# Performance work log

Hardware: AMD Instinct MI355X
Metric: run time of the kernel (lower is better)

The kernel has to match this reference:

```python
import math
import jax, jax.numpy as jnp
import numpy as np

W_BITS = 8
A_BITS = 8
N_HEADS = 16

def fake_quant(x, bits):
    # symmetric per-tensor fake quantization with straight-through estimator
    if bits >= 32:
        return x
    qmax = float(2 ** (bits - 1) - 1)
    scale = jnp.maximum(jnp.max(jnp.abs(x)) / qmax, 1e-8)
    q = jnp.round(x / scale) * scale
    return x + jax.lax.stop_gradient(q - x)

def qlinear(x, W, b):
    # QuantizeLinear: quantize activations (a_bits) and weights (w_bits), then y = x @ W^T + b
    xq = fake_quant(x, A_BITS)
    Wq = fake_quant(W, W_BITS)
    return jnp.einsum('bsd,ed->bse', xq, Wq) + b

def setup_inputs() -> dict:
    key = jax.random.key(0)
    B, S, D = 2, 2048, 1024
    ks = jax.random.split(key, 6)
    inp = {
        'hidden_states': jax.random.normal(ks[0], (B, S, D), dtype=jnp.float32),
        'attention_mask': jnp.ones((B, S), dtype=jnp.float32),
        'Wq': 0.02 * jax.random.normal(ks[1], (D, D), dtype=jnp.float32),
        'bq': jnp.zeros((D,), dtype=jnp.float32),
        'Wk': 0.02 * jax.random.normal(ks[2], (D, D), dtype=jnp.float32),
        'bk': jnp.zeros((D,), dtype=jnp.float32),
        'Wv': 0.02 * jax.random.normal(ks[3], (D, D), dtype=jnp.float32),
        'bv': jnp.zeros((D,), dtype=jnp.float32),
        'Wo': 0.02 * jax.random.normal(ks[4], (D, D), dtype=jnp.float32),
        'bo': jnp.zeros((D,), dtype=jnp.float32),
    }
    return inp

def reference(hidden_states, attention_mask, Wq, bq, Wk, bk, Wv, bv, Wo, bo):
    B, S, D = hidden_states.shape
    H = N_HEADS
    hd = D // H

    q = qlinear(hidden_states, Wq, bq).reshape(B, S, H, hd)
    k = qlinear(hidden_states, Wk, bk).reshape(B, S, H, hd)
    v = qlinear(hidden_states, Wv, bv).reshape(B, S, H, hd)

    # scores: [B, H, Sq, Sk]
    scores = jnp.einsum('bqhd,bkhd->bhqk', q, k) / math.sqrt(hd)
    mask_bias = (1.0 - attention_mask)[:, None, None, :] * -10000.0
    scores = scores + mask_bias
    probs = jax.nn.softmax(scores, axis=-1)

    attn = jnp.einsum('bhqk,bkhd->bqhd', probs, v).reshape(B, S, D)
    return qlinear(attn, Wo, bo)
```

## Files before the change

### kernel.cpp

```cpp
#include <hip/hip_runtime.h>
#include <cstddef>
#include <cstdint>

constexpr int Bb = 2, Ss = 2048, Dd = 1024, Hh = 16, HD = 64;
constexpr int Mm = Bb * Ss;

typedef int v4i __attribute__((ext_vector_type(4)));
typedef __bf16 bf16x8 __attribute__((ext_vector_type(8)));
typedef float f32x16 __attribute__((ext_vector_type(16)));

#define QPOSTMUL 0.18033688f
#define MASKBIAS -14426.950408f

__device__ __forceinline__ float qscale(float amax) {
    return fmaxf(amax / 127.0f, 1e-8f);
}

__device__ __forceinline__ unsigned short bf16rtn(float x) {
    __bf16 b = (__bf16)x;
    return __builtin_bit_cast(unsigned short, b);
}

__device__ __forceinline__ void bf16split(float x, unsigned short& hi, unsigned short& lo) {
    unsigned u = __float_as_uint(x);
    unsigned h = (u + 0x7fffu + ((u >> 16) & 1u)) >> 16;
    hi = (unsigned short)h;
    float r = x - __uint_as_float(h << 16);
    unsigned v = __float_as_uint(r);
    lo = (unsigned short)((v + 0x7fffu + ((v >> 16) & 1u)) >> 16);
}

__global__ void amax_all(const float4* __restrict__ hidden,
                         const float4* __restrict__ w0, const float4* __restrict__ w1,
                         const float4* __restrict__ w2, const float4* __restrict__ w3,
                         unsigned* __restrict__ slots) {
    const float4* src; int n4, slot, bx, nb;
    if (blockIdx.x < 256) { src = hidden; n4 = Mm * Dd / 4; slot = 0; bx = blockIdx.x; nb = 256; }
    else {
        int w = (blockIdx.x - 256) >> 4; bx = (blockIdx.x - 256) & 15; nb = 16;
        src = w == 0 ? w0 : w == 1 ? w1 : w == 2 ? w2 : w3;
        n4 = Dd * Dd / 4; slot = 1 + w;
    }
    float m = 0.f;
    for (int i = bx * blockDim.x + threadIdx.x; i < n4; i += nb * blockDim.x) {
        float4 v = src[i];
        m = fmaxf(m, fmaxf(fmaxf(fabsf(v.x), fabsf(v.y)), fmaxf(fabsf(v.z), fabsf(v.w))));
    }
    #pragma unroll
    for (int off = 32; off > 0; off >>= 1) m = fmaxf(m, __shfl_down(m, off, 64));
    __shared__ float sm[4];
    int lane = threadIdx.x & 63, wid = threadIdx.x >> 6;
    if (lane == 0) sm[wid] = m;
    __syncthreads();
    if (threadIdx.x == 0) {
        float mm = fmaxf(fmaxf(sm[0], sm[1]), fmaxf(sm[2], sm[3]));
        atomicMax(slots + slot, __float_as_uint(mm));
    }
}

__global__ void quant_all(const float* __restrict__ hidden,
                          const float* __restrict__ w0, const float* __restrict__ w1,
                          const float* __restrict__ w2, const float* __restrict__ w3,
                          const float* __restrict__ amax,
                          char* __restrict__ hq8, char* __restrict__ Wall8) {
    const float* x; char* y; int n4, slot, bx, nb;
    if (blockIdx.x < 1024) { x = hidden; y = hq8; n4 = Mm * Dd / 4; slot = 0; bx = blockIdx.x; nb = 1024; }
    else {
        int w = (blockIdx.x - 1024) >> 5; bx = (blockIdx.x - 1024) & 31; nb = 32;
        x = w == 0 ? w0 : w == 1 ? w1 : w == 2 ? w2 : w3;
        y = Wall8 + ((size_t)w << 20);
        n4 = Dd * Dd / 4; slot = 1 + w;
    }
    float s = qscale(amax[slot]);
    const float4* x4 = (const float4*)x;
    char4* y4 = (char4*)y;
    for (int i = bx * blockDim.x + threadIdx.x; i < n4; i += nb * blockDim.x) {
        float4 v = x4[i];
        char4 q;
        q.x = (char)(int)rintf(v.x / s);
        q.y = (char)(int)rintf(v.y / s);
        q.z = (char)(int)rintf(v.z / s);
        q.w = (char)(int)rintf(v.w / s);
        y4[i] = q;
    }
}

__global__ void quant_a(const float* __restrict__ x, char* __restrict__ y,
                        const float* __restrict__ amax, int n4) {
    float s = qscale(amax[0]);
    int stride = gridDim.x * blockDim.x;
    const float4* x4 = (const float4*)x;
    char4* y4 = (char4*)y;
    for (int i = blockIdx.x * blockDim.x + threadIdx.x; i < n4; i += stride) {
        float4 v = x4[i];
        char4 q;
        q.x = (char)(int)rintf(v.x / s);
        q.y = (char)(int)rintf(v.y / s);
        q.z = (char)(int)rintf(v.z / s);
        q.w = (char)(int)rintf(v.w / s);
        y4[i] = q;
    }
}

#define GLOAD_LDS16(g, l) __builtin_amdgcn_global_load_lds( \
    (const __attribute__((address_space(1))) unsigned int*)(g), \
    (__attribute__((address_space(3))) unsigned int*)(l), 16, 0, 0)

__device__ __forceinline__ void gemm_i8_core(const char* __restrict__ A, const char* __restrict__ Bw,
                                             int bm, int bn, int K, int t,
                                             char* At, char* Bt, v4i acc[4][4]) {
    const int lane = t & 63, w = t >> 6;
    const int wm = (w >> 1) * 64, wn = (w & 1) * 64;
    const int lr = lane & 15, kq = lane >> 4;
    const int rs = w * 16 + (lane >> 2);
    const int cc = lane & 3;

    for (int k0 = 0; k0 < K; k0 += 64) {
        __syncthreads();
        #pragma unroll
        for (int h = 0; h < 2; h++) {
            int r = rs + h * 64;
            int cs = cc ^ ((r >> 1) & 3);
            const char* ga = A  + (size_t)(bm + r) * K + k0 + cs * 16;
            const char* gb = Bw + (size_t)(bn + r) * K + k0 + cs * 16;
            GLOAD_LDS16(ga, At + r * 64 + cc * 16);
            GLOAD_LDS16(gb, Bt + r * 64 + cc * 16);
        }
        __syncthreads();

        v4i af[4], bf[4];
        #pragma unroll
        for (int mt = 0; mt < 4; mt++) {
            int row = wm + mt * 16 + lr;
            af[mt] = *(const v4i*)(At + row * 64 + ((kq ^ ((row >> 1) & 3)) << 4));
        }
        #pragma unroll
        for (int nt = 0; nt < 4; nt++) {
            int row = wn + nt * 16 + lr;
            bf[nt] = *(const v4i*)(Bt + row * 64 + ((kq ^ ((row >> 1) & 3)) << 4));
        }
        #pragma unroll
        for (int mt = 0; mt < 4; mt++)
            #pragma unroll
            for (int nt = 0; nt < 4; nt++)
                acc[mt][nt] = __builtin_amdgcn_mfma_i32_16x16x64_i8(af[mt], bf[nt], acc[mt][nt], 0, 0, 0);
    }
}

__global__ __launch_bounds__(256) void gemm_qkv(const char* __restrict__ A,
                                                const char* __restrict__ Wall8,
                                                const float* __restrict__ bq,
                                                const float* __restrict__ bk,
                                                const float* __restrict__ bv,
                                                const float* __restrict__ amax,
                                                unsigned short* __restrict__ qhi,
                                                unsigned short* __restrict__ qlo,
                                                unsigned short* __restrict__ khi,
                                                unsigned short* __restrict__ klo,
                                                unsigned short* __restrict__ vthi) {
    __shared__ alignas(16) char At[128 * 64];
    __shared__ alignas(16) char Bt[128 * 64];
    const int t = threadIdx.x, lane = t & 63, w = t >> 6;
    const int mat = blockIdx.x >> 3;
    const int bn = (blockIdx.x & 7) * 128, bm = blockIdx.y * 128;
    const int wm = (w >> 1) * 64, wn = (w & 1) * 64;
    const int lr = lane & 15, kq = lane >> 4;

    const v4i vzero = {0, 0, 0, 0};
    v4i acc[4][4];
    #pragma unroll
    for (int mt = 0; mt < 4; mt++)
        #pragma unroll
        for (int nt = 0; nt < 4; nt++) acc[mt][nt] = vzero;

    const char* Bw = Wall8 + ((size_t)mat << 20);
    gemm_i8_core(A, Bw, bm, bn, Dd, t, At, Bt, acc);

    const float* bias = mat == 0 ? bq : mat == 1 ? bk : bv;
    float sc = qscale(amax[0]) * qscale(amax[1 + mat]);
    float pm = (mat == 0) ? QPOSTMUL : 1.0f;

    #pragma unroll
    for (int nt = 0; nt < 4; nt++) {
        int n = bn + wn + nt * 16 + lr;
        float bv_ = bias[n];
        #pragma unroll
        for (int mt = 0; mt < 4; mt++) {
            if (mat == 2) {
                int m0 = bm + wm + mt * 16 + kq * 4;
                int b_ = m0 >> 11, s_ = m0 & 2047;
                int e = n & 63, hc = n >> 6;
                ushort4 hv;
                hv.x = bf16rtn((float)acc[mt][nt][0] * sc + bv_);
                hv.y = bf16rtn((float)acc[mt][nt][1] * sc + bv_);
                hv.z = bf16rtn((float)acc[mt][nt][2] * sc + bv_);
                hv.w = bf16rtn((float)acc[mt][nt][3] * sc + bv_);
                size_t ad = (((size_t)(b_ * Hh + hc) * 64 + e) * Ss) + s_;
                *(ushort4*)(vthi + ad) = hv;
            } else {
                unsigned short* Chi = mat == 0 ? qhi : khi;
                unsigned short* Clo = mat == 0 ? qlo : klo;
                #pragma unroll
                for (int rg = 0; rg < 4; rg++) {
                    int m = bm + wm + mt * 16 + kq * 4 + rg;
                    float val = ((float)acc[mt][nt][rg] * sc + bv_) * pm;
                    unsigned short hi, lo;
                    bf16split(val, hi, lo);
                    Chi[(size_t)m * Dd + n] = hi;
                    Clo[(size_t)m * Dd + n] = lo;
                }
            }
        }
    }
}

__global__ __launch_bounds__(256) void gemm_o(const char* __restrict__ A,
                                              const char* __restrict__ Bw,
                                              const float* __restrict__ bias,
                                              const float* __restrict__ amaxA,
                                              const float* __restrict__ amaxB,
                                              float* __restrict__ C) {
    __shared__ alignas(16) char At[128 * 64];
    __shared__ alignas(16) char Bt[128 * 64];
    const int t = threadIdx.x, lane = t & 63, w = t >> 6;
    const int bn = blockIdx.x * 128, bm = blockIdx.y * 128;
    const int wm = (w >> 1) * 64, wn = (w & 1) * 64;
    const int lr = lane & 15, kq = lane >> 4;

    const v4i vzero = {0, 0, 0, 0};
    v4i acc[4][4];
    #pragma unroll
    for (int mt = 0; mt < 4; mt++)
        #pragma unroll
        for (int nt = 0; nt < 4; nt++) acc[mt][nt] = vzero;

    gemm_i8_core(A, Bw, bm, bn, Dd, t, At, Bt, acc);

    float sc = qscale(amaxA[0]) * qscale(amaxB[0]);
    #pragma unroll
    for (int nt = 0; nt < 4; nt++) {
        int n = bn + wn + nt * 16 + lr;
        float bv_ = bias[n];
        #pragma unroll
        for (int mt = 0; mt < 4; mt++)
            #pragma unroll
            for (int rg = 0; rg < 4; rg++) {
                int m = bm + wm + mt * 16 + kq * 4 + rg;
                C[(size_t)m * Dd + n] = (float)acc[mt][nt][rg] * sc + bv_;
            }
    }
}

__global__ __launch_bounds__(256) void attn_mfma(
    const unsigned short* __restrict__ qhi, const unsigned short* __restrict__ qlo,
    const unsigned short* __restrict__ khi, const unsigned short* __restrict__ klo,
    const unsigned short* __restrict__ vthi,
    const float* __restrict__ mask, float* __restrict__ Ob, unsigned* __restrict__ amax_out) {
    __shared__ alignas(16) unsigned short KsHi[64][72], KsLo[64][72], VsHi[64][72];
    __shared__ alignas(16) unsigned short Pw[4][32][72];
    __shared__ float mbias[64];
    __shared__ float wred[4];

    const int t = threadIdx.x, lane = t & 63, wq = t >> 6;
    const int ln31 = lane & 31, h5 = lane >> 5;
    const int b = blockIdx.z, h = blockIdx.y, q0 = blockIdx.x * 128;

    bf16x8 qfh[4], qfl[4];
    {
        int qrow = q0 + wq * 32 + ln31;
        const unsigned short* qb_ = qhi + ((size_t)(b * Ss + qrow)) * Dd + h * 64 + h5 * 8;
        const unsigned short* ql_ = qlo + ((size_t)(b * Ss + qrow)) * Dd + h * 64 + h5 * 8;
        #pragma unroll
        for (int c = 0; c < 4; c++) {
            qfh[c] = *(const bf16x8*)(qb_ + c * 16);
            qfl[c] = *(const bf16x8*)(ql_ + c * 16);
        }
    }

    f32x16 o0 = 0.f, o1 = 0.f;
    float lp[16];
    #pragma unroll
    for (int r = 0; r < 16; r++) lp[r] = 0.f;

    for (int k0 = 0; k0 < Ss; k0 += 64) {
        __syncthreads();
        {
            int r = t >> 2, cp = (t & 3) * 2;
            const unsigned short* gk  = khi + ((size_t)(b * Ss + k0 + r)) * Dd + h * 64 + cp * 8;
            const unsigned short* gkl = klo + ((size_t)(b * Ss + k0 + r)) * Dd + h * 64 + cp * 8;
            const unsigned short* gv  = vthi + (((size_t)(b * Hh + h) * 64 + r)) * Ss + k0 + cp * 8;
            *(int4*)&KsHi[r][cp * 8]     = *(const int4*)gk;
            *(int4*)&KsHi[r][cp * 8 + 8] = *(const int4*)(gk + 8);
            *(int4*)&KsLo[r][cp * 8]     = *(const int4*)gkl;
            *(int4*)&KsLo[r][cp * 8 + 8] = *(const int4*)(gkl + 8);
            *(int4*)&VsHi[r][cp * 8]     = *(const int4*)gv;
            *(int4*)&VsHi[r][cp * 8 + 8] = *(const int4*)(gv + 8);
            if (t < 64) mbias[t] = (1.0f - mask[b * Ss + k0 + t]) * MASKBIAS;
        }
        __syncthreads();

        f32x16 sc0 = 0.f, sc1 = 0.f;
        #pragma unroll
        for (int c = 0; c < 4; c++) {
            bf16x8 kh0 = *(const bf16x8*)&KsHi[ln31][c * 16 + h5 * 8];
            bf16x8 kl0 = *(const bf16x8*)&KsLo[ln31][c * 16 + h5 * 8];
            bf16x8 kh1 = *(const bf16x8*)&KsHi[32 + ln31][c * 16 + h5 * 8];
            bf16x8 kl1 = *(const bf16x8*)&KsLo[32 + ln31][c * 16 + h5 * 8];
            sc0 = __builtin_amdgcn_mfma_f32_32x32x16_bf16(qfl[c], kh0, sc0, 0, 0, 0);
            sc0 = __builtin_amdgcn_mfma_f32_32x32x16_bf16(qfh[c], kl0, sc0, 0, 0, 0);
            sc0 = __builtin_amdgcn_mfma_f32_32x32x16_bf16(qfh[c], kh0, sc0, 0, 0, 0);
            sc1 = __builtin_amdgcn_mfma_f32_32x32x16_bf16(qfl[c], kh1, sc1, 0, 0, 0);
            sc1 = __builtin_amdgcn_mfma_f32_32x32x16_bf16(qfh[c], kl1, sc1, 0, 0, 0);
            sc1 = __builtin_amdgcn_mfma_f32_32x32x16_bf16(qfh[c], kh1, sc1, 0, 0, 0);
        }

        float mb0 = mbias[ln31], mb1 = mbias[32 + ln31];
        #pragma unroll
        for (int r = 0; r < 16; r++) {
            float p0 = __builtin_amdgcn_exp2f(sc0[r] + mb0);
            float p1 = __builtin_amdgcn_exp2f(sc1[r] + mb1);
            lp[r] += p0 + p1;
            int row = (r & 3) + 8 * (r >> 2) + 4 * h5;
            Pw[wq][row][ln31] = bf16rtn(p0);
            Pw[wq][row][32 + ln31] = bf16rtn(p1);
        }

        #pragma unroll
        for (int c = 0; c < 4; c++) {
            bf16x8 pf = *(const bf16x8*)&Pw[wq][ln31][c * 16 + h5 * 8];
            bf16x8 vh0 = *(const bf16x8*)&VsHi[ln31][c * 16 + h5 * 8];
            bf16x8 vh1 = *(const bf16x8*)&VsHi[32 + ln31][c * 16 + h5 * 8];
            o0 = __builtin_amdgcn_mfma_f32_32x32x16_bf16(pf, vh0, o0, 0, 0, 0);
            o1 = __builtin_amdgcn_mfma_f32_32x32x16_bf16(pf, vh1, o1, 0, 0, 0);
        }
    }

    float lmax = 0.f;
    #pragma unroll
    for (int r = 0; r < 16; r++) {
        float l = lp[r];
        #pragma unroll
        for (int off = 1; off < 32; off <<= 1) l += __shfl_xor(l, off, 32);
        float inv = 1.0f / l;
        int row = q0 + wq * 32 + (r & 3) + 8 * (r >> 2) + 4 * h5;
        size_t ro = ((size_t)(b * Ss + row)) * Dd + h * 64;
        float v0 = o0[r] * inv, v1 = o1[r] * inv;
        Ob[ro + ln31] = v0;
        Ob[ro + 32 + ln31] = v1;
        lmax = fmaxf(lmax, fmaxf(fabsf(v0), fabsf(v1)));
    }
    #pragma unroll
    for (int off = 32; off > 0; off >>= 1) lmax = fmaxf(lmax, __shfl_xor(lmax, off, 64));
    if (lane == 0) wred[wq] = lmax;
    __syncthreads();
    if (t == 0) {
        float m = fmaxf(fmaxf(wred[0], wred[1]), fmaxf(wred[2], wred[3]));
        atomicMax(amax_out, __float_as_uint(m));
    }
}

extern "C" void kernel_launch(void* const* d_in, const int* in_sizes, int n_in,
                              void* d_out, int out_size, void* d_ws, size_t ws_size,
                              hipStream_t stream) {
    const float* hidden = (const float*)d_in[0];
    const float* mask   = (const float*)d_in[1];
    const float* Wq = (const float*)d_in[2];
    const float* bq = (const float*)d_in[3];
    const float* Wk = (const float*)d_in[4];
    const float* bk = (const float*)d_in[5];
    const float* Wv = (const float*)d_in[6];
    const float* bv = (const float*)d_in[7];
    const float* Wo = (const float*)d_in[8];
    const float* bo = (const float*)d_in[9];
    float* out = (float*)d_out;

    char* ws = (char*)d_ws;
    float* scal = (float*)ws;
    size_t off = 1024;
    const size_t szH8 = (size_t)Mm * Dd;
    const size_t szHb = (size_t)Mm * Dd * sizeof(unsigned short);
    const size_t szHf = (size_t)Mm * Dd * sizeof(float);
    char* hq8   = ws + off; off += szH8;
    char* Wall8 = ws + off; off += 4u << 20;
    char* aq8   = ws + off; off += szH8;
    unsigned short* qhi  = (unsigned short*)(ws + off); off += szHb;
    unsigned short* qlo  = (unsigned short*)(ws + off); off += szHb;
    unsigned short* khi  = (unsigned short*)(ws + off); off += szHb;
    unsigned short* klo  = (unsigned short*)(ws + off); off += szHb;
    unsigned short* vthi = (unsigned short*)(ws + off); off += szHb;
    float* ab = (float*)(ws + off); off += szHf;

    hipMemsetAsync(scal, 0, 64, stream);

    amax_all<<<320, 256, 0, stream>>>((const float4*)hidden, (const float4*)Wq,
                                      (const float4*)Wk, (const float4*)Wv, (const float4*)Wo,
                                      (unsigned*)scal);
    quant_all<<<1152, 256, 0, stream>>>(hidden, Wq, Wk, Wv, Wo, scal, hq8, Wall8);

    gemm_qkv<<<dim3(24, 32), 256, 0, stream>>>(hq8, Wall8, bq, bk, bv, scal,
                                               qhi, qlo, khi, klo, vthi);

    attn_mfma<<<dim3(Ss / 128, Hh, Bb), 256, 0, stream>>>(qhi, qlo, khi, klo, vthi,
                                                          mask, ab, (unsigned*)(scal + 5));

    quant_a<<<1024, 256, 0, stream>>>(ab, aq8, scal + 5, Mm * Dd / 4);

    gemm_o<<<dim3(8, 32), 256, 0, stream>>>(aq8, Wall8 + (3u << 20), bo,
                                            scal + 5, scal + 4, out);
}
```

Before: 253.7 us.

## Shrink GEMM tiles to 64x64, prefetch K/V in attention, pack P stores

Both int8 GEMMs move from 128x128 to 64x64 block tiles with a 2x2 MFMA grid per wave, giving four times as many blocks so the GPU is better filled, at the cost of less data reuse per block. The attention kernel now loads the next K/V/mask tile into registers while computing on the current one. K rows are permuted in LDS, and the probability tile is written as packed bf16 pairs, halving the number of LDS stores. The amax kernel also gets more blocks for the hidden-state reduction.

```diff
diff --git a/kernel.cpp b/kernel.cpp
--- a/kernel.cpp
+++ b/kernel.cpp
@@ -19,6 +19,13 @@
 __device__ __forceinline__ unsigned short bf16rtn(float x) {
     __bf16 b = (__bf16)x;
     return __builtin_bit_cast(unsigned short, b);
+}
+
+__device__ __forceinline__ unsigned pack_bf16x2(float a, float b) {
+    unsigned ua = __float_as_uint(a), ub = __float_as_uint(b);
+    unsigned ha = (ua + 0x7fffu + ((ua >> 16) & 1u)) >> 16;
+    unsigned hb = (ub + 0x7fffu + ((ub >> 16) & 1u)) & 0xffff0000u;
+    return ha | hb;
 }
 
 __device__ __forceinline__ void bf16split(float x, unsigned short& hi, unsigned short& lo) {
@@ -35,9 +42,9 @@
                          const float4* __restrict__ w2, const float4* __restrict__ w3,
                          unsigned* __restrict__ slots) {
     const float4* src; int n4, slot, bx, nb;
-    if (blockIdx.x < 256) { src = hidden; n4 = Mm * Dd / 4; slot = 0; bx = blockIdx.x; nb = 256; }
+    if (blockIdx.x < 448) { src = hidden; n4 = Mm * Dd / 4; slot = 0; bx = blockIdx.x; nb = 448; }
     else {
-        int w = (blockIdx.x - 256) >> 4; bx = (blockIdx.x - 256) & 15; nb = 16;
+        int w = (blockIdx.x - 448) >> 4; bx = (blockIdx.x - 448) & 15; nb = 16;
         src = w == 0 ? w0 : w == 1 ? w1 : w == 2 ? w2 : w3;
         n4 = Dd * Dd / 4; slot = 1 + w;
     }
@@ -106,43 +113,37 @@
     (const __attribute__((address_space(1))) unsigned int*)(g), \
     (__attribute__((address_space(3))) unsigned int*)(l), 16, 0, 0)
 
-__device__ __forceinline__ void gemm_i8_core(const char* __restrict__ A, const char* __restrict__ Bw,
-                                             int bm, int bn, int K, int t,
-                                             char* At, char* Bt, v4i acc[4][4]) {
+__device__ __forceinline__ void gemm64_core(const char* __restrict__ A, const char* __restrict__ Bw,
+                                            int bm, int bn, int K, int t,
+                                            char* At, char* Bt, v4i acc[2][2]) {
     const int lane = t & 63, w = t >> 6;
-    const int wm = (w >> 1) * 64, wn = (w & 1) * 64;
+    const int wm = (w >> 1) * 32, wn = (w & 1) * 32;
     const int lr = lane & 15, kq = lane >> 4;
-    const int rs = w * 16 + (lane >> 2);
-    const int cc = lane & 3;
+    const int rs = t >> 2;
+    const int cc = t & 3;
+    const int cs = cc ^ ((rs >> 1) & 3);
 
     for (int k0 = 0; k0 < K; k0 += 64) {
         __syncthreads();
-        #pragma unroll
-        for (int h = 0; h < 2; h++) {
-            int r = rs + h * 64;
-            int cs = cc ^ ((r >> 1) & 3);
-            const char* ga = A  + (size_t)(bm + r) * K + k0 + cs * 16;
-            const char* gb = Bw + (size_t)(bn + r) * K + k0 + cs * 16;
-            GLOAD_LDS16(ga, At + r * 64 + cc * 16);
-            GLOAD_LDS16(gb, Bt + r * 64 + cc * 16);
-        }
+        GLOAD_LDS16(A  + (size_t)(bm + rs) * K + k0 + cs * 16, At + rs * 64 + cc * 16);
+        GLOAD_LDS16(Bw + (size_t)(bn + rs) * K + k0 + cs * 16, Bt + rs * 64 + cc * 16);
         __syncthreads();
 
-        v4i af[4], bf[4];
-        #pragma unroll
-        for (int mt = 0; mt < 4; mt++) {
+        v4i af[2], bf[2];
+        #pragma unroll
+        for (int mt = 0; mt < 2; mt++) {
             int row = wm + mt * 16 + lr;
             af[mt] = *(const v4i*)(At + row * 64 + ((kq ^ ((row >> 1) & 3)) << 4));
         }
         #pragma unroll
-        for (int nt = 0; nt < 4; nt++) {
+        for (int nt = 0; nt < 2; nt++) {
             int row = wn + nt * 16 + lr;
             bf[nt] = *(const v4i*)(Bt + row * 64 + ((kq ^ ((row >> 1) & 3)) << 4));
         }
         #pragma unroll
-        for (int mt = 0; mt < 4; mt++)
+        for (int mt = 0; mt < 2; mt++)
             #pragma unroll
-            for (int nt = 0; nt < 4; nt++)
+            for (int nt = 0; nt < 2; nt++)
                 acc[mt][nt] = __builtin_amdgcn_mfma_i32_16x16x64_i8(af[mt], bf[nt], acc[mt][nt], 0, 0, 0);
     }
 }
@@ -158,34 +159,30 @@
                                                 unsigned short* __restrict__ khi,
                                                 unsigned short* __restrict__ klo,
                                                 unsigned short* __restrict__ vthi) {
-    __shared__ alignas(16) char At[128 * 64];
-    __shared__ alignas(16) char Bt[128 * 64];
+    __shared__ alignas(16) char At[64 * 64];
+    __shared__ alignas(16) char Bt[64 * 64];
     const int t = threadIdx.x, lane = t & 63, w = t >> 6;
-    const int mat = blockIdx.x >> 3;
-    const int bn = (blockIdx.x & 7) * 128, bm = blockIdx.y * 128;
-    const int wm = (w >> 1) * 64, wn = (w & 1) * 64;
+    const int mat = blockIdx.x >> 4;
+    const int bn = (blockIdx.x & 15) * 64, bm = blockIdx.y * 64;
+    const int wm = (w >> 1) * 32, wn = (w & 1) * 32;
     const int lr = lane & 15, kq = lane >> 4;
 
     const v4i vzero = {0, 0, 0, 0};
-    v4i acc[4][4];
-    #pragma unroll
-    for (int mt = 0; mt < 4; mt++)
-        #pragma unroll
-        for (int nt = 0; nt < 4; nt++) acc[mt][nt] = vzero;
+    v4i acc[2][2] = {{vzero, vzero}, {vzero, vzero}};
 
     const char* Bw = Wall8 + ((size_t)mat << 20);
-    gemm_i8_core(A, Bw, bm, bn, Dd, t, At, Bt, acc);
+    gemm64_core(A, Bw, bm, bn, Dd, t, At, Bt, acc);
 
     const float* bias = mat == 0 ? bq : mat == 1 ? bk : bv;
     float sc = qscale(amax[0]) * qscale(amax[1 + mat]);
     float pm = (mat == 0) ? QPOSTMUL : 1.0f;
 
     #pragma unroll
-    for (int nt = 0; nt < 4; nt++) {
+    for (int nt = 0; nt < 2; nt++) {
         int n = bn + wn + nt * 16 + lr;
         float bv_ = bias[n];
         #pragma unroll
-        for (int mt = 0; mt < 4; mt++) {
+        for (int mt = 0; mt < 2; mt++) {
             if (mat == 2) {
                 int m0 = bm + wm + mt * 16 + kq * 4;
                 int b_ = m0 >> 11, s_ = m0 & 2047;
@@ -220,29 +217,25 @@
                                               const float* __restrict__ amaxA,
                                               const float* __restrict__ amaxB,
                                               float* __restrict__ C) {
-    __shared__ alignas(16) char At[128 * 64];
-    __shared__ alignas(16) char Bt[128 * 64];
+    __shared__ alignas(16) char At[64 * 64];
+    __shared__ alignas(16) char Bt[64 * 64];
     const int t = threadIdx.x, lane = t & 63, w = t >> 6;
-    const int bn = blockIdx.x * 128, bm = blockIdx.y * 128;
-    const int wm = (w >> 1) * 64, wn = (w & 1) * 64;
+    const int bn = blockIdx.x * 64, bm = blockIdx.y * 64;
+    const int wm = (w >> 1) * 32, wn = (w & 1) * 32;
     const int lr = lane & 15, kq = lane >> 4;
 
     const v4i vzero = {0, 0, 0, 0};
-    v4i acc[4][4];
-    #pragma unroll
-    for (int mt = 0; mt < 4; mt++)
-        #pragma unroll
-        for (int nt = 0; nt < 4; nt++) acc[mt][nt] = vzero;
-
-    gemm_i8_core(A, Bw, bm, bn, Dd, t, At, Bt, acc);
+    v4i acc[2][2] = {{vzero, vzero}, {vzero, vzero}};
+
+    gemm64_core(A, Bw, bm, bn, Dd, t, At, Bt, acc);
 
     float sc = qscale(amaxA[0]) * qscale(amaxB[0]);
     #pragma unroll
-    for (int nt = 0; nt < 4; nt++) {
+    for (int nt = 0; nt < 2; nt++) {
         int n = bn + wn + nt * 16 + lr;
         float bv_ = bias[n];
         #pragma unroll
-        for (int mt = 0; mt < 4; mt++)
+        for (int mt = 0; mt < 2; mt++)
             #pragma unroll
             for (int rg = 0; rg < 4; rg++) {
                 int m = bm + wm + mt * 16 + kq * 4 + rg;
@@ -257,7 +250,7 @@
     const unsigned short* __restrict__ vthi,
     const float* __restrict__ mask, float* __restrict__ Ob, unsigned* __restrict__ amax_out) {
     __shared__ alignas(16) unsigned short KsHi[64][72], KsLo[64][72], VsHi[64][72];
-    __shared__ alignas(16) unsigned short Pw[4][32][72];
+    __shared__ alignas(16) unsigned PwU[4][32][36];
     __shared__ float mbias[64];
     __shared__ float wred[4];
 
@@ -277,27 +270,36 @@
         }
     }
 
+    const int srow = t >> 2, cp = (t & 3) * 2;
+    const int rho = (srow >> 1) + (srow & 1) * 32;
+    int4 pk0, pk1, pl0, pl1, pv0, pv1; float pmask = 1.f;
+    auto prefetch = [&](int k0) {
+        const unsigned short* gk  = khi + ((size_t)(b * Ss + k0 + srow)) * Dd + h * 64 + cp * 8;
+        const unsigned short* gkl = klo + ((size_t)(b * Ss + k0 + srow)) * Dd + h * 64 + cp * 8;
+        const unsigned short* gv  = vthi + (((size_t)(b * Hh + h) * 64 + srow)) * Ss + k0 + cp * 8;
+        pk0 = *(const int4*)gk;  pk1 = *(const int4*)(gk + 8);
+        pl0 = *(const int4*)gkl; pl1 = *(const int4*)(gkl + 8);
+        pv0 = *(const int4*)gv;  pv1 = *(const int4*)(gv + 8);
+        if (t < 64) pmask = mask[b * Ss + k0 + t];
+    };
+
     f32x16 o0 = 0.f, o1 = 0.f;
     float lp[16];
     #pragma unroll
     for (int r = 0; r < 16; r++) lp[r] = 0.f;
 
+    prefetch(0);
     for (int k0 = 0; k0 < Ss; k0 += 64) {
         __syncthreads();
-        {
-            int r = t >> 2, cp = (t & 3) * 2;
-            const unsigned short* gk  = khi + ((size_t)(b * Ss + k0 + r)) * Dd + h * 64 + cp * 8;
-            const unsigned short* gkl = klo + ((size_t)(b * Ss + k0 + r)) * Dd + h * 64 + cp * 8;
-            const unsigned short* gv  = vthi + (((size_t)(b * Hh + h) * 64 + r)) * Ss + k0 + cp * 8;
-            *(int4*)&KsHi[r][cp * 8]     = *(const int4*)gk;
-            *(int4*)&KsHi[r][cp * 8 + 8] = *(const int4*)(gk + 8);
-            *(int4*)&KsLo[r][cp * 8]     = *(const int4*)gkl;
-            *(int4*)&KsLo[r][cp * 8 + 8] = *(const int4*)(gkl + 8);
-            *(int4*)&VsHi[r][cp * 8]     = *(const int4*)gv;
-            *(int4*)&VsHi[r][cp * 8 + 8] = *(const int4*)(gv + 8);
-            if (t < 64) mbias[t] = (1.0f - mask[b * Ss + k0 + t]) * MASKBIAS;
-        }
+        *(int4*)&KsHi[rho][cp * 8]      = pk0;
+        *(int4*)&KsHi[rho][cp * 8 + 8]  = pk1;
+        *(int4*)&KsLo[rho][cp * 8]      = pl0;
+        *(int4*)&KsLo[rho][cp * 8 + 8]  = pl1;
+        *(int4*)&VsHi[srow][cp * 8]     = pv0;
+        *(int4*)&VsHi[srow][cp * 8 + 8] = pv1;
+        if (t < 64) mbias[t] = (1.0f - pmask) * MASKBIAS;
         __syncthreads();
+        if (k0 + 64 < Ss) prefetch(k0 + 64);
 
         f32x16 sc0 = 0.f, sc1 = 0.f;
         #pragma unroll
@@ -314,20 +316,19 @@
             sc1 = __builtin_amdgcn_mfma_f32_32x32x16_bf16(qfh[c], kh1, sc1, 0, 0, 0);
         }
 
-        float mb0 = mbias[ln31], mb1 = mbias[32 + ln31];
+        float mb0 = mbias[2 * ln31], mb1 = mbias[2 * ln31 + 1];
         #pragma unroll
         for (int r = 0; r < 16; r++) {
             float p0 = __builtin_amdgcn_exp2f(sc0[r] + mb0);
             float p1 = __builtin_amdgcn_exp2f(sc1[r] + mb1);
             lp[r] += p0 + p1;
             int row = (r & 3) + 8 * (r >> 2) + 4 * h5;
-            Pw[wq][row][ln31] = bf16rtn(p0);
-            Pw[wq][row][32 + ln31] = bf16rtn(p1);
+            PwU[wq][row][ln31] = pack_bf16x2(p0, p1);
         }
 
         #pragma unroll
         for (int c = 0; c < 4; c++) {
-            bf16x8 pf = *(const bf16x8*)&Pw[wq][ln31][c * 16 + h5 * 8];
+            bf16x8 pf = *(const bf16x8*)((const unsigned short*)&PwU[wq][ln31][0] + c * 16 + h5 * 8);
             bf16x8 vh0 = *(const bf16x8*)&VsHi[ln31][c * 16 + h5 * 8];
             bf16x8 vh1 = *(const bf16x8*)&VsHi[32 + ln31][c * 16 + h5 * 8];
             o0 = __builtin_amdgcn_mfma_f32_32x32x16_bf16(pf, vh0, o0, 0, 0, 0);
@@ -392,12 +393,12 @@
 
     hipMemsetAsync(scal, 0, 64, stream);
 
-    amax_all<<<320, 256, 0, stream>>>((const float4*)hidden, (const float4*)Wq,
+    amax_all<<<512, 256, 0, stream>>>((const float4*)hidden, (const float4*)Wq,
                                       (const float4*)Wk, (const float4*)Wv, (const float4*)Wo,
                                       (unsigned*)scal);
     quant_all<<<1152, 256, 0, stream>>>(hidden, Wq, Wk, Wv, Wo, scal, hq8, Wall8);
 
-    gemm_qkv<<<dim3(24, 32), 256, 0, stream>>>(hq8, Wall8, bq, bk, bv, scal,
+    gemm_qkv<<<dim3(48, 64), 256, 0, stream>>>(hq8, Wall8, bq, bk, bv, scal,
                                                qhi, qlo, khi, klo, vthi);
 
     attn_mfma<<<dim3(Ss / 128, Hh, Bb), 256, 0, stream>>>(qhi, qlo, khi, klo, vthi,
@@ -405,6 +406,6 @@
 
     quant_a<<<1024, 256, 0, stream>>>(ab, aq8, scal + 5, Mm * Dd / 4);
 
-    gemm_o<<<dim3(8, 32), 256, 0, stream>>>(aq8, Wall8 + (3u << 20), bo,
-                                            scal + 5, scal + 4, out);
-}
+    gemm_o<<<dim3(16, 64), 256, 0, stream>>>(aq8, Wall8 + (3u << 20), bo,
+                                             scal + 5, scal + 4, out);
+}
```

Result: slower. 258.9 us (+2.0%).

## Drop bf16 hi/lo split for Q/K, prefetch K/V, retile output GEMM

Applied to the files above, without the earlier changes.

Q and K are now stored as a single bf16 value instead of a hi/lo pair, so QK^T takes one MFMA per chunk instead of three and the qlo/klo buffers and their traffic go away. The attention loop prefetches the next K/V tile into registers while computing, and packs the two P values per lane into one 32-bit shared-memory store using an interleaved K row order. The output GEMM moves to 128x64 tiles so it launches twice as many blocks, and the amax kernel gets more blocks for the hidden tensor. The cost is lower score precision, which could push results past the tolerance around the 8-bit rounding in the final quantization.

```diff
diff --git a/kernel.cpp b/kernel.cpp
--- a/kernel.cpp
+++ b/kernel.cpp
@@ -21,13 +21,11 @@
     return __builtin_bit_cast(unsigned short, b);
 }
 
-__device__ __forceinline__ void bf16split(float x, unsigned short& hi, unsigned short& lo) {
-    unsigned u = __float_as_uint(x);
-    unsigned h = (u + 0x7fffu + ((u >> 16) & 1u)) >> 16;
-    hi = (unsigned short)h;
-    float r = x - __uint_as_float(h << 16);
-    unsigned v = __float_as_uint(r);
-    lo = (unsigned short)((v + 0x7fffu + ((v >> 16) & 1u)) >> 16);
+__device__ __forceinline__ unsigned pack_bf16x2(float a, float b) {
+    unsigned ua = __float_as_uint(a), ub = __float_as_uint(b);
+    unsigned ha = (ua + 0x7fffu + ((ua >> 16) & 1u)) >> 16;
+    unsigned hb = (ub + 0x7fffu + ((ub >> 16) & 1u)) & 0xffff0000u;
+    return ha | hb;
 }
 
 __global__ void amax_all(const float4* __restrict__ hidden,
@@ -35,9 +33,9 @@
                          const float4* __restrict__ w2, const float4* __restrict__ w3,
                          unsigned* __restrict__ slots) {
     const float4* src; int n4, slot, bx, nb;
-    if (blockIdx.x < 256) { src = hidden; n4 = Mm * Dd / 4; slot = 0; bx = blockIdx.x; nb = 256; }
+    if (blockIdx.x < 448) { src = hidden; n4 = Mm * Dd / 4; slot = 0; bx = blockIdx.x; nb = 448; }
     else {
-        int w = (blockIdx.x - 256) >> 4; bx = (blockIdx.x - 256) & 15; nb = 16;
+        int w = (blockIdx.x - 448) >> 4; bx = (blockIdx.x - 448) & 15; nb = 16;
         src = w == 0 ? w0 : w == 1 ? w1 : w == 2 ? w2 : w3;
         n4 = Dd * Dd / 4; slot = 1 + w;
     }
@@ -106,7 +104,7 @@
     (const __attribute__((address_space(1))) unsigned int*)(g), \
     (__attribute__((address_space(3))) unsigned int*)(l), 16, 0, 0)
 
-__device__ __forceinline__ void gemm_i8_core(const char* __restrict__ A, const char* __restrict__ Bw,
+__device__ __forceinline__ void gemm128_core(const char* __restrict__ A, const char* __restrict__ Bw,
                                              int bm, int bn, int K, int t,
                                              char* At, char* Bt, v4i acc[4][4]) {
     const int lane = t & 63, w = t >> 6;
@@ -121,10 +119,8 @@
         for (int h = 0; h < 2; h++) {
             int r = rs + h * 64;
             int cs = cc ^ ((r >> 1) & 3);
-            const char* ga = A  + (size_t)(bm + r) * K + k0 + cs * 16;
-            const char* gb = Bw + (size_t)(bn + r) * K + k0 + cs * 16;
-            GLOAD_LDS16(ga, At + r * 64 + cc * 16);
-            GLOAD_LDS16(gb, Bt + r * 64 + cc * 16);
+            GLOAD_LDS16(A  + (size_t)(bm + r) * K + k0 + cs * 16, At + r * 64 + cc * 16);
+            GLOAD_LDS16(Bw + (size_t)(bn + r) * K + k0 + cs * 16, Bt + r * 64 + cc * 16);
         }
         __syncthreads();
 
@@ -153,11 +149,9 @@
                                                 const float* __restrict__ bk,
                                                 const float* __restrict__ bv,
                                                 const float* __restrict__ amax,
-                                                unsigned short* __restrict__ qhi,
-                                                unsigned short* __restrict__ qlo,
-                                                unsigned short* __restrict__ khi,
-                                                unsigned short* __restrict__ klo,
-                                                unsigned short* __restrict__ vthi) {
+                                                unsigned short* __restrict__ qb16,
+                                                unsigned short* __restrict__ kb16,
+                                                unsigned short* __restrict__ vt16) {
     __shared__ alignas(16) char At[128 * 64];
     __shared__ alignas(16) char Bt[128 * 64];
     const int t = threadIdx.x, lane = t & 63, w = t >> 6;
@@ -174,7 +168,7 @@
         for (int nt = 0; nt < 4; nt++) acc[mt][nt] = vzero;
 
     const char* Bw = Wall8 + ((size_t)mat << 20);
-    gemm_i8_core(A, Bw, bm, bn, Dd, t, At, Bt, acc);
+    gemm128_core(A, Bw, bm, bn, Dd, t, At, Bt, acc);
 
     const float* bias = mat == 0 ? bq : mat == 1 ? bk : bv;
     float sc = qscale(amax[0]) * qscale(amax[1 + mat]);
@@ -196,18 +190,13 @@
                 hv.z = bf16rtn((float)acc[mt][nt][2] * sc + bv_);
                 hv.w = bf16rtn((float)acc[mt][nt][3] * sc + bv_);
                 size_t ad = (((size_t)(b_ * Hh + hc) * 64 + e) * Ss) + s_;
-                *(ushort4*)(vthi + ad) = hv;
+                *(ushort4*)(vt16 + ad) = hv;
             } else {
-                unsigned short* Chi = mat == 0 ? qhi : khi;
-                unsigned short* Clo = mat == 0 ? qlo : klo;
+                unsigned short* C = mat == 0 ? qb16 : kb16;
                 #pragma unroll
                 for (int rg = 0; rg < 4; rg++) {
                     int m = bm + wm + mt * 16 + kq * 4 + rg;
-                    float val = ((float)acc[mt][nt][rg] * sc + bv_) * pm;
-                    unsigned short hi, lo;
-                    bf16split(val, hi, lo);
-                    Chi[(size_t)m * Dd + n] = hi;
-                    Clo[(size_t)m * Dd + n] = lo;
+                    C[(size_t)m * Dd + n] = bf16rtn(((float)acc[mt][nt][rg] * sc + bv_) * pm);
                 }
             }
         }
@@ -221,24 +210,48 @@
                                               const float* __restrict__ amaxB,
                                               float* __restrict__ C) {
     __shared__ alignas(16) char At[128 * 64];
-    __shared__ alignas(16) char Bt[128 * 64];
+    __shared__ alignas(16) char Bt[64 * 64];
     const int t = threadIdx.x, lane = t & 63, w = t >> 6;
-    const int bn = blockIdx.x * 128, bm = blockIdx.y * 128;
-    const int wm = (w >> 1) * 64, wn = (w & 1) * 64;
+    const int bn = blockIdx.x * 64, bm = blockIdx.y * 128;
+    const int wm = (w >> 1) * 64, wn = (w & 1) * 32;
     const int lr = lane & 15, kq = lane >> 4;
+    const int rs = t >> 2, cc = t & 3;
+    const int cs = cc ^ ((rs >> 1) & 3);
+    const int rs2 = rs + 64, cs2 = cc ^ ((rs2 >> 1) & 3);
 
     const v4i vzero = {0, 0, 0, 0};
-    v4i acc[4][4];
-    #pragma unroll
-    for (int mt = 0; mt < 4; mt++)
-        #pragma unroll
-        for (int nt = 0; nt < 4; nt++) acc[mt][nt] = vzero;
-
-    gemm_i8_core(A, Bw, bm, bn, Dd, t, At, Bt, acc);
+    v4i acc[4][2];
+    #pragma unroll
+    for (int mt = 0; mt < 4; mt++) { acc[mt][0] = vzero; acc[mt][1] = vzero; }
+
+    for (int k0 = 0; k0 < Dd; k0 += 64) {
+        __syncthreads();
+        GLOAD_LDS16(A  + (size_t)(bm + rs)  * Dd + k0 + cs  * 16, At + rs  * 64 + cc * 16);
+        GLOAD_LDS16(A  + (size_t)(bm + rs2) * Dd + k0 + cs2 * 16, At + rs2 * 64 + cc * 16);
+        GLOAD_LDS16(Bw + (size_t)(bn + rs)  * Dd + k0 + cs  * 16, Bt + rs  * 64 + cc * 16);
+        __syncthreads();
+
+        v4i af[4], bf[2];
+        #pragma unroll
+        for (int mt = 0; mt < 4; mt++) {
+            int row = wm + mt * 16 + lr;
+            af[mt] = *(const v4i*)(At + row * 64 + ((kq ^ ((row >> 1) & 3)) << 4));
+        }
+        #pragma unroll
+        for (int nt = 0; nt < 2; nt++) {
+            int row = wn + nt * 16 + lr;
+            bf[nt] = *(const v4i*)(Bt + row * 64 + ((kq ^ ((row >> 1) & 3)) << 4));
+        }
+        #pragma unroll
+        for (int mt = 0; mt < 4; mt++)
+            #pragma unroll
+            for (int nt = 0; nt < 2; nt++)
+                acc[mt][nt] = __builtin_amdgcn_mfma_i32_16x16x64_i8(af[mt], bf[nt], acc[mt][nt], 0, 0, 0);
+    }
 
     float sc = qscale(amaxA[0]) * qscale(amaxB[0]);
     #pragma unroll
-    for (int nt = 0; nt < 4; nt++) {
+    for (int nt = 0; nt < 2; nt++) {
         int n = bn + wn + nt * 16 + lr;
         float bv_ = bias[n];
         #pragma unroll
@@ -252,12 +265,11 @@
 }
 
 __global__ __launch_bounds__(256) void attn_mfma(
-    const unsigned short* __restrict__ qhi, const unsigned short* __restrict__ qlo,
-    const unsigned short* __restrict__ khi, const unsigned short* __restrict__ klo,
-    const unsigned short* __restrict__ vthi,
+    const unsigned short* __restrict__ qb16, const unsigned short* __restrict__ kb16,
+    const unsigned short* __restrict__ vt16,
     const float* __restrict__ mask, float* __restrict__ Ob, unsigned* __restrict__ amax_out) {
-    __shared__ alignas(16) unsigned short KsHi[64][72], KsLo[64][72], VsHi[64][72];
-    __shared__ alignas(16) unsigned short Pw[4][32][72];
+    __shared__ alignas(16) unsigned short KsHi[64][72], VsHi[64][72];
+    __shared__ alignas(16) unsigned PwU[4][32][36];
     __shared__ float mbias[64];
     __shared__ float wred[4];
 
@@ -265,69 +277,63 @@
     const int ln31 = lane & 31, h5 = lane >> 5;
     const int b = blockIdx.z, h = blockIdx.y, q0 = blockIdx.x * 128;
 
-    bf16x8 qfh[4], qfl[4];
+    bf16x8 qf[4];
     {
         int qrow = q0 + wq * 32 + ln31;
-        const unsigned short* qb_ = qhi + ((size_t)(b * Ss + qrow)) * Dd + h * 64 + h5 * 8;
-        const unsigned short* ql_ = qlo + ((size_t)(b * Ss + qrow)) * Dd + h * 64 + h5 * 8;
-        #pragma unroll
-        for (int c = 0; c < 4; c++) {
-            qfh[c] = *(const bf16x8*)(qb_ + c * 16);
-            qfl[c] = *(const bf16x8*)(ql_ + c * 16);
-        }
-    }
+        const unsigned short* qb_ = qb16 + ((size_t)(b * Ss + qrow)) * Dd + h * 64 + h5 * 8;
+        #pragma unroll
+        for (int c = 0; c < 4; c++) qf[c] = *(const bf16x8*)(qb_ + c * 16);
+    }
+
+    const int srow = t >> 2, cp = (t & 3) * 2;
+    const int rho = (srow >> 1) + (srow & 1) * 32;
+    int4 pk0, pk1, pv0, pv1; float pmask = 1.f;
+    auto prefetch = [&](int k0) {
+        const unsigned short* gk = kb16 + ((size_t)(b * Ss + k0 + srow)) * Dd + h * 64 + cp * 8;
+        const unsigned short* gv = vt16 + (((size_t)(b * Hh + h) * 64 + srow)) * Ss + k0 + cp * 8;
+        pk0 = *(const int4*)gk; pk1 = *(const int4*)(gk + 8);
+        pv0 = *(const int4*)gv; pv1 = *(const int4*)(gv + 8);
+        if (t < 64) pmask = mask[b * Ss + k0 + t];
+    };
 
     f32x16 o0 = 0.f, o1 = 0.f;
     float lp[16];
     #pragma unroll
     for (int r = 0; r < 16; r++) lp[r] = 0.f;
 
+    prefetch(0);
     for (int k0 = 0; k0 < Ss; k0 += 64) {
         __syncthreads();
-        {
-            int r = t >> 2, cp = (t & 3) * 2;
-            const unsigned short* gk  = khi + ((size_t)(b * Ss + k0 + r)) * Dd + h * 64 + cp * 8;
-            const unsigned short* gkl = klo + ((size_t)(b * Ss + k0 + r)) * Dd + h * 64 + cp * 8;
-            const unsigned short* gv  = vthi + (((size_t)(b * Hh + h) * 64 + r)) * Ss + k0 + cp * 8;
-            *(int4*)&KsHi[r][cp * 8]     = *(const int4*)gk;
-            *(int4*)&KsHi[r][cp * 8 + 8] = *(const int4*)(gk + 8);
-            *(int4*)&KsLo[r][cp * 8]     = *(const int4*)gkl;
-            *(int4*)&KsLo[r][cp * 8 + 8] = *(const int4*)(gkl + 8);
-            *(int4*)&VsHi[r][cp * 8]     = *(const int4*)gv;
-            *(int4*)&VsHi[r][cp * 8 + 8] = *(const int4*)(gv + 8);
-            if (t < 64) mbias[t] = (1.0f - mask[b * Ss + k0 + t]) * MASKBIAS;
-        }
-        __syncthreads();
+        *(int4*)&KsHi[rho][cp * 8]      = pk0;
+        *(int4*)&KsHi[rho][cp * 8 + 8]  = pk1;
+        *(int4*)&VsHi[srow][cp * 8]     = pv0;
+        *(int4*)&VsHi[srow][cp * 8 + 8] = pv1;
+        if (t < 64) mbias[t] = (1.0f - pmask) * MASKBIAS;
+        __syncthreads();
+        if (k0 + 64 < Ss) prefetch(k0 + 64);
 
         f32x16 sc0 = 0.f, sc1 = 0.f;
         #pragma unroll
         for (int c = 0; c < 4; c++) {
             bf16x8 kh0 = *(const bf16x8*)&KsHi[ln31][c * 16 + h5 * 8];
-            bf16x8 kl0 = *(const bf16x8*)&KsLo[ln31][c * 16 + h5 * 8];
             bf16x8 kh1 = *(const bf16x8*)&KsHi[32 + ln31][c * 16 + h5 * 8];
-            bf16x8 kl1 = *(const bf16x8*)&KsLo[32 + ln31][c * 16 + h5 * 8];
-            sc0 = __builtin_amdgcn_mfma_f32_32x32x16_bf16(qfl[c], kh0, sc0, 0, 0, 0);
-            sc0 = __builtin_amdgcn_mfma_f32_32x32x16_bf16(qfh[c], kl0, sc0, 0, 0, 0);
-            sc0 = __builtin_amdgcn_mfma_f32_32x32x16_bf16(qfh[c], kh0, sc0, 0, 0, 0);
-            sc1 = __builtin_amdgcn_mfma_f32_32x32x16_bf16(qfl[c], kh1, sc1, 0, 0, 0);
-            sc1 = __builtin_amdgcn_mfma_f32_32x32x16_bf16(qfh[c], kl1, sc1, 0, 0, 0);
-            sc1 = __builtin_amdgcn_mfma_f32_32x32x16_bf16(qfh[c], kh1, sc1, 0, 0, 0);
-        }
-
-        float mb0 = mbias[ln31], mb1 = mbias[32 + ln31];
+            sc0 = __builtin_amdgcn_mfma_f32_32x32x16_bf16(qf[c], kh0, sc0, 0, 0, 0);
+            sc1 = __builtin_amdgcn_mfma_f32_32x32x16_bf16(qf[c], kh1, sc1, 0, 0, 0);
+        }
+
+        float mb0 = mbias[2 * ln31], mb1 = mbias[2 * ln31 + 1];
         #pragma unroll
         for (int r = 0; r < 16; r++) {
             float p0 = __builtin_amdgcn_exp2f(sc0[r] + mb0);
             float p1 = __builtin_amdgcn_exp2f(sc1[r] + mb1);
             lp[r] += p0 + p1;
             int row = (r & 3) + 8 * (r >> 2) + 4 * h5;
-            Pw[wq][row][ln31] = bf16rtn(p0);
-            Pw[wq][row][32 + ln31] = bf16rtn(p1);
+            PwU[wq][row][ln31] = pack_bf16x2(p0, p1);
         }
 
         #pragma unroll
         for (int c = 0; c < 4; c++) {
-            bf16x8 pf = *(const bf16x8*)&Pw[wq][ln31][c * 16 + h5 * 8];
+            bf16x8 pf = *(const bf16x8*)((const unsigned short*)&PwU[wq][ln31][0] + c * 16 + h5 * 8);
             bf16x8 vh0 = *(const bf16x8*)&VsHi[ln31][c * 16 + h5 * 8];
             bf16x8 vh1 = *(const bf16x8*)&VsHi[32 + ln31][c * 16 + h5 * 8];
             o0 = __builtin_amdgcn_mfma_f32_32x32x16_bf16(pf, vh0, o0, 0, 0, 0);
@@ -383,28 +389,26 @@
     char* hq8   = ws + off; off += szH8;
     char* Wall8 = ws + off; off += 4u << 20;
     char* aq8   = ws + off; off += szH8;
-    unsigned short* qhi  = (unsigned short*)(ws + off); off += szHb;
-    unsigned short* qlo  = (unsigned short*)(ws + off); off += szHb;
-    unsigned short* khi  = (unsigned short*)(ws + off); off += szHb;
-    unsigned short* klo  = (unsigned short*)(ws + off); off += szHb;
-    unsigned short* vthi = (unsigned short*)(ws + off); off += szHb;
+    unsigned short* qb16 = (unsigned short*)(ws + off); off += szHb;
+    unsigned short* kb16 = (unsigned short*)(ws + off); off += szHb;
+    unsigned short* vt16 = (unsigned short*)(ws + off); off += szHb;
     float* ab = (float*)(ws + off); off += szHf;
 
     hipMemsetAsync(scal, 0, 64, stream);
 
-    amax_all<<<320, 256, 0, stream>>>((const float4*)hidden, (const float4*)Wq,
+    amax_all<<<512, 256, 0, stream>>>((const float4*)hidden, (const float4*)Wq,
                                       (const float4*)Wk, (const float4*)Wv, (const float4*)Wo,
                                       (unsigned*)scal);
     quant_all<<<1152, 256, 0, stream>>>(hidden, Wq, Wk, Wv, Wo, scal, hq8, Wall8);
 
     gemm_qkv<<<dim3(24, 32), 256, 0, stream>>>(hq8, Wall8, bq, bk, bv, scal,
-                                               qhi, qlo, khi, klo, vthi);
-
-    attn_mfma<<<dim3(Ss / 128, Hh, Bb), 256, 0, stream>>>(qhi, qlo, khi, klo, vthi,
+                                               qb16, kb16, vt16);
+
+    attn_mfma<<<dim3(Ss / 128, Hh, Bb), 256, 0, stream>>>(qb16, kb16, vt16,
                                                           mask, ab, (unsigned*)(scal + 5));
 
     quant_a<<<1024, 256, 0, stream>>>(ab, aq8, scal + 5, Mm * Dd / 4);
 
-    gemm_o<<<dim3(8, 32), 256, 0, stream>>>(aq8, Wall8 + (3u << 20), bo,
-                                            scal + 5, scal + 4, out);
-}
+    gemm_o<<<dim3(16, 32), 256, 0, stream>>>(aq8, Wall8 + (3u << 20), bo,
+                                             scal + 5, scal + 4, out);
+}
```

Measured after the change: 237.8 us. 6.2% less time.
